# Kernel optimization log

Hardware: AMD Instinct MI355X
Metric: run time of the kernel (lower is better)

The kernel has to match this reference:

```python
import jax, jax.numpy as jnp
import numpy as np

DIM = 256
L = 16            # block_size (query rows per leaf block)
H = 8             # num_heads
D = DIM // H      # head_dim = 32
KC = L + 1        # key count: L leaf nodes + 1 block (mean) node, layout '16x17'
B = 2
N = 32768         # multiple of L -> no padding path
NB = N // L       # 2048 blocks
SCALE = D ** -0.5


def setup_inputs() -> dict:
    key = jax.random.key(0)
    ks = jax.random.split(key, 8)
    x = jax.random.normal(ks[0], (B, N, DIM), jnp.float32)
    attn_mask = jax.random.randint(ks[1], (NB, L, KC), 0, 2, dtype=jnp.int32)
    ar = jnp.arange(L)
    attn_mask = attn_mask.at[:, ar, ar].set(1)  # self always visible -> no all-masked rows
    edge_feats = jax.random.normal(ks[2], (NB, L, KC, 4), jnp.float32)
    s = DIM ** -0.5
    Wqkv = jax.random.normal(ks[3], (3 * DIM, DIM), jnp.float32) * s
    bqkv = jnp.zeros((3 * DIM,), jnp.float32)
    Wproj = jax.random.normal(ks[4], (DIM, DIM), jnp.float32) * s
    bproj = jnp.zeros((DIM,), jnp.float32)
    Wgate = jax.random.normal(ks[5], (H, 4), jnp.float32) * 0.01  # nn.init.normal_(std=0.01)
    bgate = jnp.zeros((H,), jnp.float32)
    return {"x": x, "attn_mask": attn_mask, "edge_feats": edge_feats,
            "Wqkv": Wqkv, "bqkv": bqkv, "Wproj": Wproj, "bproj": bproj,
            "Wgate": Wgate, "bgate": bgate}


def reference(x, attn_mask, edge_feats, Wqkv, bqkv, Wproj, bproj, Wgate, bgate):
    # x: [B, N, C] -> blocks [B, NB, L, C]
    x_blk = x.reshape(B, NB, L, DIM)
    block_node = x_blk.mean(axis=2, keepdims=True)           # virtual block node
    kv = jnp.concatenate([x_blk, block_node], axis=2)         # [B, NB, KC, C]

    # qkv projections (slice of the fused Linear; rows are independent so math is identical)
    q = x_blk @ Wqkv[:DIM].T + bqkv[:DIM]
    k = kv @ Wqkv[DIM:2 * DIM].T + bqkv[DIM:2 * DIM]
    v = kv @ Wqkv[2 * DIM:].T + bqkv[2 * DIM:]
    q = q.reshape(B, NB, L, H, D)
    k = k.reshape(B, NB, KC, H, D)
    v = v.reshape(B, NB, KC, H, D)

    scores = jnp.einsum('bnqhd,bnkhd->bnqkh', q, k) * SCALE   # [B, NB, L, KC, H]

    # physics bias: zero out + set channel 3 = 1 for block node column and self (diagonal)
    ar = jnp.arange(L)
    unit = jnp.array([0.0, 0.0, 0.0, 1.0], edge_feats.dtype)
    bias = edge_feats.at[:, :, L, :].set(unit)                # block-node column
    bias = bias.at[:, ar, ar, :].set(unit)                    # self bias on diagonal
    bias = jnp.broadcast_to(bias[None], (B, NB, L, KC, 4))    # expand over batch

    scores = scores + bias[..., 3:4]

    mask0 = (attn_mask[None] == 0)[..., None]                 # [1, NB, L, KC, 1]
    scores = jnp.where(mask0, -jnp.inf, scores)
    attn = jax.nn.softmax(scores, axis=3)

    gate = jnp.einsum('bnqkf,hf->bnqkh', bias, Wgate) + bgate  # edge-conditioned gate
    gate = jnp.where(mask0, 0.0, gate)

    combined = attn + gate
    out = jnp.einsum('bnqkh,bnkhd->bnqhd', combined, v).reshape(B, N, DIM)
    return out @ Wproj.T + bproj
```

## Files before the change

### kernel.cpp

```cpp
#include <hip/hip_runtime.h>
#include <cstdint>
#include <cstddef>

#define B_SZ 2
#define N_SEQ 32768
#define NB 2048
#define HD 32
#define LQ 16
#define KCNT 17
#define M_ROWS 65536
#define SCALE_F 0.17677669529663687f

typedef __attribute__((ext_vector_type(8))) short sv8;
typedef __attribute__((ext_vector_type(4))) short sv4;
typedef __attribute__((ext_vector_type(4))) float f4;

__device__ __forceinline__ short f2bf(float f) {
  unsigned u = __builtin_bit_cast(unsigned, f);
  u = (u + 0x7FFFu + ((u >> 16) & 1u)) >> 16;
  return (short)u;
}
__device__ __forceinline__ float bf2f(short s) {
  unsigned u = ((unsigned)(unsigned short)s) << 16;
  return __builtin_bit_cast(float, u);
}
__device__ __forceinline__ void gload16(const void* g, void* l) {
  __builtin_amdgcn_global_load_lds(
      (const __attribute__((address_space(1))) unsigned int*)g,
      (__attribute__((address_space(3))) unsigned int*)l, 16, 0, 0);
}
__device__ __forceinline__ f4 mfma16(sv8 a, sv8 b, f4 c) {
  return __builtin_amdgcn_mfma_f32_16x16x32_bf16(a, b, c, 0, 0, 0);
}

__global__ __launch_bounds__(256) void cast_w(
    const float* __restrict__ wq, const float* __restrict__ wp,
    short* __restrict__ W1, short* __restrict__ WP1) {
  const int i = blockIdx.x * 256 + threadIdx.x;
  const float* src;
  short* dst;
  int off;
  if (i < 49152) { src = wq; dst = W1; off = i; }
  else if (i < 49152 + 16384) { src = wp; dst = WP1; off = i - 49152; }
  else return;
  float4 v = ((const float4*)src)[off];
  sv4 h = {f2bf(v.x), f2bf(v.y), f2bf(v.z), f2bf(v.w)};
  *(sv4*)&dst[(size_t)off * 4] = h;
}

__global__ __launch_bounds__(256) void gemm_fused_qkv(
    const float* __restrict__ Xf, const short* __restrict__ B1,
    const float* __restrict__ bias, short* __restrict__ Qbf,
    short* __restrict__ Kbf, short* __restrict__ Vbf) {
  __shared__ __align__(16) short Ahs[2][128][32];
  __shared__ __align__(16) short Bhs[2][128][32];
  const int tid = threadIdx.x;
  const int w = tid >> 6, l = tid & 63;
  const int wm = w >> 1, wn = w & 1;
  const int bid = blockIdx.x;
  const int chunkc = (6 * 512) >> 3;
  const int lbid = (bid & 7) * chunkc + (bid >> 3);
  const int nti = lbid % 6, mti = lbid / 6;
  const int m0 = mti * 128, n0 = nti * 128;
  const int lr = l >> 2, lc = (l & 3) * 8;
  const int fr = l & 15, kg = (l >> 4) * 8;
  const int ar = w * 32 + lr, ac = lc;
  f4 acc[4][4] = {};

#pragma unroll
  for (int i = 0; i < 2; ++i)
    gload16(B1 + (size_t)(n0 + w * 32 + i * 16 + lr) * 256 + lc,
            (void*)&Bhs[0][w * 32 + i * 16][0]);
#pragma unroll
  for (int i = 0; i < 2; ++i) {
    const float* ap = Xf + (size_t)(m0 + ar + i * 16) * 256 + ac;
    float4 x0 = *(const float4*)ap;
    float4 x1 = *(const float4*)(ap + 4);
    sv8 o;
    o[0] = f2bf(x0.x); o[1] = f2bf(x0.y); o[2] = f2bf(x0.z); o[3] = f2bf(x0.w);
    o[4] = f2bf(x1.x); o[5] = f2bf(x1.y); o[6] = f2bf(x1.z); o[7] = f2bf(x1.w);
    *(sv8*)&Ahs[0][ar + i * 16][ac] = o;
  }
  asm volatile("s_waitcnt vmcnt(0) lgkmcnt(0)" ::: "memory");
  __builtin_amdgcn_s_barrier();

  for (int s = 0; s < 8; ++s) {
    const int cb = s & 1, nbuf = cb ^ 1;
    float4 pa0[2], pa1[2];
    if (s < 7) {
      const int sk = (s + 1) * 32;
#pragma unroll
      for (int i = 0; i < 2; ++i)
        gload16(B1 + (size_t)(n0 + w * 32 + i * 16 + lr) * 256 + sk + lc,
                (void*)&Bhs[nbuf][w * 32 + i * 16][0]);
#pragma unroll
      for (int i = 0; i < 2; ++i) {
        const float* ap = Xf + (size_t)(m0 + ar + i * 16) * 256 + sk + ac;
        pa0[i] = *(const float4*)ap;
        pa1[i] = *(const float4*)(ap + 4);
      }
    }
    sv8 fa[4], fb[4];
#pragma unroll
    for (int t = 0; t < 4; ++t) {
      fa[t] = *(const sv8*)&Ahs[cb][wm * 64 + t * 16 + fr][kg];
      fb[t] = *(const sv8*)&Bhs[cb][wn * 64 + t * 16 + fr][kg];
    }
#pragma unroll
    for (int mt = 0; mt < 4; ++mt)
#pragma unroll
      for (int nt2 = 0; nt2 < 4; ++nt2)
        acc[mt][nt2] = mfma16(fa[mt], fb[nt2], acc[mt][nt2]);
    if (s < 7) {
#pragma unroll
      for (int i = 0; i < 2; ++i) {
        sv8 o;
        o[0] = f2bf(pa0[i].x); o[1] = f2bf(pa0[i].y);
        o[2] = f2bf(pa0[i].z); o[3] = f2bf(pa0[i].w);
        o[4] = f2bf(pa1[i].x); o[5] = f2bf(pa1[i].y);
        o[6] = f2bf(pa1[i].z); o[7] = f2bf(pa1[i].w);
        *(sv8*)&Ahs[nbuf][ar + i * 16][ac] = o;
      }
    }
    asm volatile("s_waitcnt vmcnt(0) lgkmcnt(0)" ::: "memory");
    __builtin_amdgcn_s_barrier();
  }

  short* dst = (nti < 2) ? Qbf : ((nti < 4) ? Kbf : Vbf);
  const int r0 = (l >> 4) * 4;
#pragma unroll
  for (int mt = 0; mt < 4; ++mt)
#pragma unroll
    for (int nt2 = 0; nt2 < 4; ++nt2) {
      const int n = n0 + wn * 64 + nt2 * 16 + fr;
      const float bv = bias[n];
      const int nn = n & 255;
      const size_t mb = (size_t)(m0 + wm * 64 + mt * 16 + r0);
#pragma unroll
      for (int j = 0; j < 4; ++j)
        dst[(mb + j) * 256 + nn] = f2bf(acc[mt][nt2][j] + bv);
    }
}

__global__ __launch_bounds__(256) void gemm_proj1(
    const short* __restrict__ A1, const short* __restrict__ B1,
    const float* __restrict__ bias, float* __restrict__ C) {
  __shared__ __align__(16) short Ahs[2][128][32];
  __shared__ __align__(16) short Bhs[2][128][32];
  const int tid = threadIdx.x;
  const int w = tid >> 6, l = tid & 63;
  const int wm = w >> 1, wn = w & 1;
  const int bid = blockIdx.x;
  const int chunkc = (2 * 512) >> 3;
  const int lbid = (bid & 7) * chunkc + (bid >> 3);
  const int nti = lbid % 2, mti = lbid / 2;
  const int m0 = mti * 128, n0 = nti * 128;
  const int lr = l >> 2, lc = (l & 3) * 8;
  const int fr = l & 15, kg = (l >> 4) * 8;
  f4 acc[4][4] = {};
#pragma unroll
  for (int i = 0; i < 2; ++i) {
    const int row = w * 32 + i * 16;
    gload16(A1 + (size_t)(m0 + row + lr) * 256 + lc, (void*)&Ahs[0][row][0]);
    gload16(B1 + (size_t)(n0 + row + lr) * 256 + lc, (void*)&Bhs[0][row][0]);
  }
  asm volatile("s_waitcnt vmcnt(0)" ::: "memory");
  __builtin_amdgcn_s_barrier();
  int cur = 0;
  for (int s = 0; s < 8; ++s) {
    if (s < 7) {
      const int sk = (s + 1) * 32;
#pragma unroll
      for (int i = 0; i < 2; ++i) {
        const int row = w * 32 + i * 16;
        gload16(A1 + (size_t)(m0 + row + lr) * 256 + sk + lc,
                (void*)&Ahs[cur ^ 1][row][0]);
        gload16(B1 + (size_t)(n0 + row + lr) * 256 + sk + lc,
                (void*)&Bhs[cur ^ 1][row][0]);
      }
    }
    if (s > 0) {
      if (s < 7) asm volatile("s_waitcnt vmcnt(4)" ::: "memory");
      else asm volatile("s_waitcnt vmcnt(0)" ::: "memory");
      __builtin_amdgcn_s_barrier();
    }
    sv8 fa[4], fb[4];
#pragma unroll
    for (int t = 0; t < 4; ++t) {
      fa[t] = *(const sv8*)&Ahs[cur][wm * 64 + t * 16 + fr][kg];
      fb[t] = *(const sv8*)&Bhs[cur][wn * 64 + t * 16 + fr][kg];
    }
#pragma unroll
    for (int mt = 0; mt < 4; ++mt)
#pragma unroll
      for (int nt2 = 0; nt2 < 4; ++nt2)
        acc[mt][nt2] = mfma16(fa[mt], fb[nt2], acc[mt][nt2]);
    asm volatile("s_waitcnt lgkmcnt(0)" ::: "memory");
    __builtin_amdgcn_s_barrier();
    cur ^= 1;
  }
  const int r0 = (l >> 4) * 4;
#pragma unroll
  for (int mt = 0; mt < 4; ++mt)
#pragma unroll
    for (int nt2 = 0; nt2 < 4; ++nt2) {
      const int n = n0 + wn * 64 + nt2 * 16 + fr;
      const float bv = bias[n];
      const size_t mb = (size_t)(m0 + wm * 64 + mt * 16 + r0);
#pragma unroll
      for (int j = 0; j < 4; ++j) C[(mb + j) * 256 + n] = acc[mt][nt2][j] + bv;
    }
}

__global__ __launch_bounds__(256, 5) void attn_v7(
    const short* __restrict__ Qb, const short* __restrict__ Kb,
    const short* __restrict__ Vb, const int* __restrict__ amask,
    const float* __restrict__ efeat, const float* __restrict__ Wgate,
    const float* __restrict__ bgate, short* __restrict__ AO) {
  __shared__ __align__(16) short Kl[16 * 264];
  __shared__ __align__(16) short Vl[16 * 264];
  __shared__ __align__(16) short Ol[16 * 264];
  __shared__ float4 Es[LQ * KCNT];
  __shared__ int Ms[LQ * KCNT];

  const int tid = threadIdx.x, g = blockIdx.x;
  const int b = g >> 11, nb = g & (NB - 1);
  const size_t tok0 = (size_t)(b * N_SEQ + nb * LQ);
  const int w = tid >> 6, l = tid & 63;
  const int ln = l & 15, lg = l >> 4;
  const f4 fzero = {0.f, 0.f, 0.f, 0.f};

  sv8 qf[2];
#pragma unroll
  for (int hh = 0; hh < 2; ++hh) {
    const int h = w * 2 + hh;
    qf[hh] = *(const sv8*)(Qb + (tok0 + ln) * 256 + h * 32 + lg * 8);
  }

#pragma unroll
  for (int i = 0; i < 2; ++i) {
    const int f = tid + i * 256;
    const int t = f >> 5, c8 = (f & 31) * 8;
    *(sv8*)&Kl[t * 264 + c8] = *(const sv8*)(Kb + (tok0 + t) * 256 + c8);
    *(sv8*)&Vl[t * 264 + c8] = *(const sv8*)(Vb + (tok0 + t) * 256 + c8);
  }
  {
    const float4* esrc = (const float4*)(efeat + (size_t)nb * LQ * KCNT * 4);
    const int* msrc = amask + (size_t)nb * LQ * KCNT;
    Es[tid] = esrc[tid];
    Ms[tid] = msrc[tid];
    if (tid < LQ * KCNT - 256) {
      Es[256 + tid] = esrc[256 + tid];
      Ms[256 + tid] = msrc[256 + tid];
    }
  }
  __syncthreads();

  const int q = ln;
#pragma unroll
  for (int hh = 0; hh < 2; ++hh) {
    const int h = w * 2 + hh;
    sv8 ka = *(const sv8*)&Kl[ln * 264 + h * 32 + lg * 8];
    f4 sr = mfma16(ka, qf[hh], fzero);

    const float wg0 = Wgate[h * 4], wg1 = Wgate[h * 4 + 1];
    const float wg2 = Wgate[h * 4 + 2], wg3 = Wgate[h * 4 + 3];
    const float bg = bgate[h];

    float rs = sr[0] + sr[1] + sr[2] + sr[3];
    rs += __shfl_xor(rs, 16);
    rs += __shfl_xor(rs, 32);

    float s_[4], gt_[4];
    int vis_[4];
#pragma unroll
    for (int j = 0; j < 4; ++j) {
      const int kc = lg * 4 + j;
      float e0, e1, e2, e3;
      if (kc == q) { e0 = e1 = e2 = 0.f; e3 = 1.f; }
      else { float4 e = Es[q * KCNT + kc]; e0 = e.x; e1 = e.y; e2 = e.z; e3 = e.w; }
      const int m = Ms[q * KCNT + kc];
      vis_[j] = m;
      s_[j] = sr[j] * SCALE_F + e3;
      gt_[j] = m ? (e0 * wg0 + e1 * wg1 + e2 * wg2 + e3 * wg3 + bg) : 0.f;
    }
    const int m16 = Ms[q * KCNT + 16];
    const float s16 = rs * 0.0625f * SCALE_F + 1.0f;

    float mx = -1e30f;
#pragma unroll
    for (int j = 0; j < 4; ++j)
      if (vis_[j]) mx = fmaxf(mx, s_[j]);
    mx = fmaxf(mx, __shfl_xor(mx, 16));
    mx = fmaxf(mx, __shfl_xor(mx, 32));
    if (m16) mx = fmaxf(mx, s16);

    float p_[4], den = 0.f;
#pragma unroll
    for (int j = 0; j < 4; ++j) {
      p_[j] = vis_[j] ? __expf(s_[j] - mx) : 0.f;
      den += p_[j];
    }
    den += __shfl_xor(den, 16);
    den += __shfl_xor(den, 32);
    const float p16 = m16 ? __expf(s16 - mx) : 0.f;
    den += p16;
    const float inv = 1.f / den;
    const float gt16 = m16 ? (wg3 + bg) : 0.f;
    const float cb16 = (p16 * inv + gt16) * 0.0625f;
    float pc[4];
#pragma unroll
    for (int j = 0; j < 4; ++j) pc[j] = p_[j] * inv + gt_[j] + cb16;

    sv8 pa;
#pragma unroll
    for (int e = 0; e < 8; ++e) {
      const int kc = lg * 8 + e;
      const int src = ((kc >> 2) << 4) | q;
      const float v0 = __shfl(pc[e & 3], src);
      pa[e] = (kc < 16) ? f2bf(v0) : (short)0;
    }

#pragma unroll
    for (int t = 0; t < 2; ++t) {
      sv8 vb;
#pragma unroll
      for (int e = 0; e < 8; ++e) {
        const int vr = (lg * 8 + e) & 15;
        vb[e] = Vl[vr * 264 + h * 32 + t * 16 + ln];
      }
      f4 oacc = mfma16(pa, vb, fzero);
#pragma unroll
      for (int j = 0; j < 4; ++j)
        Ol[(lg * 4 + j) * 264 + h * 32 + t * 16 + ln] = f2bf(oacc[j]);
    }
  }
  __syncthreads();

#pragma unroll
  for (int i = 0; i < 2; ++i) {
    const int f = tid + i * 256;
    const int t = f >> 5, c8 = (f & 31) * 8;
    *(sv8*)(AO + (tok0 + t) * 256 + c8) = *(const sv8*)&Ol[t * 264 + c8];
  }
}

extern "C" void kernel_launch(void* const* d_in, const int* in_sizes, int n_in,
                              void* d_out, int out_size, void* d_ws, size_t ws_size,
                              hipStream_t stream) {
  const float* x = (const float*)d_in[0];
  const int* amask = (const int*)d_in[1];
  const float* efeat = (const float*)d_in[2];
  const float* Wqkv = (const float*)d_in[3];
  const float* bqkv = (const float*)d_in[4];
  const float* Wproj = (const float*)d_in[5];
  const float* bproj = (const float*)d_in[6];
  const float* Wgate = (const float*)d_in[7];
  const float* bgate = (const float*)d_in[8];
  float* out = (float*)d_out;

  char* ws = (char*)d_ws;
  const size_t QB_SZ = (size_t)M_ROWS * 256 * 2;
  const size_t W1_SZ = (size_t)768 * 256 * 2;
  const size_t WP1_SZ = (size_t)256 * 256 * 2;
  if (ws_size < 4 * QB_SZ + W1_SZ + WP1_SZ) return;

  short* Qbf = (short*)ws;
  short* Kbf = (short*)(ws + QB_SZ);
  short* Vbf = (short*)(ws + 2 * QB_SZ);
  short* AOh = (short*)(ws + 3 * QB_SZ);
  short* W1 = (short*)(ws + 4 * QB_SZ);
  short* WP1 = (short*)(ws + 4 * QB_SZ + W1_SZ);

  cast_w<<<dim3((49152 + 16384 + 255) / 256), 256, 0, stream>>>(Wqkv, Wproj,
                                                                W1, WP1);
  gemm_fused_qkv<<<dim3(6 * 512), 256, 0, stream>>>(x, W1, bqkv, Qbf, Kbf, Vbf);
  attn_v7<<<dim3(B_SZ * NB), 256, 0, stream>>>(Qbf, Kbf, Vbf, amask, efeat,
                                               Wgate, bgate, AOh);
  gemm_proj1<<<dim3(2 * 512), 256, 0, stream>>>(AOh, WP1, bproj, out);
}
```

Before: 138.5 us.

## Pre-cast x to bf16 and stage QKV GEMM epilogue through swizzled LDS

Converts x to bf16 in a separate cast pass so the QKV GEMM can load both operands with direct global-to-LDS loads. It also adds a finer-grained wait on outstanding loads, and writes outputs through an XOR-swizzled LDS tile so the global stores are coalesced 16-byte rows. The aim is to remove the per-stage float-to-bf16 conversion and register staging from the GEMM main loop and to avoid scattered 2-byte stores. The cost is an extra full pass that reads x in fp32 and writes a bf16 copy, plus more workspace. Since x is re-read six times by the GEMM, the extra pass may be partly offset by halved reads.

```diff
diff --git a/kernel.cpp b/kernel.cpp
--- a/kernel.cpp
+++ b/kernel.cpp
@@ -33,27 +33,28 @@
   return __builtin_amdgcn_mfma_f32_16x16x32_bf16(a, b, c, 0, 0, 0);
 }
 
-__global__ __launch_bounds__(256) void cast_w(
-    const float* __restrict__ wq, const float* __restrict__ wp,
+__global__ __launch_bounds__(256) void cast_all(
+    const float* __restrict__ x, const float* __restrict__ wq,
+    const float* __restrict__ wp, short* __restrict__ X1,
     short* __restrict__ W1, short* __restrict__ WP1) {
   const int i = blockIdx.x * 256 + threadIdx.x;
   const float* src;
   short* dst;
   int off;
-  if (i < 49152) { src = wq; dst = W1; off = i; }
-  else if (i < 49152 + 16384) { src = wp; dst = WP1; off = i - 49152; }
+  if (i < 4194304) { src = x; dst = X1; off = i; }
+  else if (i < 4194304 + 49152) { src = wq; dst = W1; off = i - 4194304; }
+  else if (i < 4194304 + 49152 + 16384) { src = wp; dst = WP1; off = i - 4194304 - 49152; }
   else return;
   float4 v = ((const float4*)src)[off];
   sv4 h = {f2bf(v.x), f2bf(v.y), f2bf(v.z), f2bf(v.w)};
   *(sv4*)&dst[(size_t)off * 4] = h;
 }
 
-__global__ __launch_bounds__(256) void gemm_fused_qkv(
-    const float* __restrict__ Xf, const short* __restrict__ B1,
+__global__ __launch_bounds__(256) void gemm_bf_qkv(
+    const short* __restrict__ A1, const short* __restrict__ B1,
     const float* __restrict__ bias, short* __restrict__ Qbf,
     short* __restrict__ Kbf, short* __restrict__ Vbf) {
-  __shared__ __align__(16) short Ahs[2][128][32];
-  __shared__ __align__(16) short Bhs[2][128][32];
+  __shared__ __align__(16) short LB[2][2][128][32];
   const int tid = threadIdx.x;
   const int w = tid >> 6, l = tid & 63;
   const int wm = w >> 1, wn = w & 1;
@@ -64,82 +65,72 @@
   const int m0 = mti * 128, n0 = nti * 128;
   const int lr = l >> 2, lc = (l & 3) * 8;
   const int fr = l & 15, kg = (l >> 4) * 8;
-  const int ar = w * 32 + lr, ac = lc;
   f4 acc[4][4] = {};
-
-#pragma unroll
-  for (int i = 0; i < 2; ++i)
-    gload16(B1 + (size_t)(n0 + w * 32 + i * 16 + lr) * 256 + lc,
-            (void*)&Bhs[0][w * 32 + i * 16][0]);
 #pragma unroll
   for (int i = 0; i < 2; ++i) {
-    const float* ap = Xf + (size_t)(m0 + ar + i * 16) * 256 + ac;
-    float4 x0 = *(const float4*)ap;
-    float4 x1 = *(const float4*)(ap + 4);
-    sv8 o;
-    o[0] = f2bf(x0.x); o[1] = f2bf(x0.y); o[2] = f2bf(x0.z); o[3] = f2bf(x0.w);
-    o[4] = f2bf(x1.x); o[5] = f2bf(x1.y); o[6] = f2bf(x1.z); o[7] = f2bf(x1.w);
-    *(sv8*)&Ahs[0][ar + i * 16][ac] = o;
-  }
-  asm volatile("s_waitcnt vmcnt(0) lgkmcnt(0)" ::: "memory");
+    const int row = w * 32 + i * 16;
+    gload16(A1 + (size_t)(m0 + row + lr) * 256 + lc, (void*)&LB[0][0][row][0]);
+    gload16(B1 + (size_t)(n0 + row + lr) * 256 + lc, (void*)&LB[0][1][row][0]);
+  }
+  asm volatile("s_waitcnt vmcnt(0)" ::: "memory");
   __builtin_amdgcn_s_barrier();
-
+  int cur = 0;
   for (int s = 0; s < 8; ++s) {
-    const int cb = s & 1, nbuf = cb ^ 1;
-    float4 pa0[2], pa1[2];
     if (s < 7) {
       const int sk = (s + 1) * 32;
 #pragma unroll
-      for (int i = 0; i < 2; ++i)
-        gload16(B1 + (size_t)(n0 + w * 32 + i * 16 + lr) * 256 + sk + lc,
-                (void*)&Bhs[nbuf][w * 32 + i * 16][0]);
-#pragma unroll
       for (int i = 0; i < 2; ++i) {
-        const float* ap = Xf + (size_t)(m0 + ar + i * 16) * 256 + sk + ac;
-        pa0[i] = *(const float4*)ap;
-        pa1[i] = *(const float4*)(ap + 4);
+        const int row = w * 32 + i * 16;
+        gload16(A1 + (size_t)(m0 + row + lr) * 256 + sk + lc,
+                (void*)&LB[cur ^ 1][0][row][0]);
+        gload16(B1 + (size_t)(n0 + row + lr) * 256 + sk + lc,
+                (void*)&LB[cur ^ 1][1][row][0]);
       }
     }
+    if (s > 0) {
+      if (s < 7) asm volatile("s_waitcnt vmcnt(4)" ::: "memory");
+      else asm volatile("s_waitcnt vmcnt(0)" ::: "memory");
+      __builtin_amdgcn_s_barrier();
+    }
     sv8 fa[4], fb[4];
 #pragma unroll
     for (int t = 0; t < 4; ++t) {
-      fa[t] = *(const sv8*)&Ahs[cb][wm * 64 + t * 16 + fr][kg];
-      fb[t] = *(const sv8*)&Bhs[cb][wn * 64 + t * 16 + fr][kg];
+      fa[t] = *(const sv8*)&LB[cur][0][wm * 64 + t * 16 + fr][kg];
+      fb[t] = *(const sv8*)&LB[cur][1][wn * 64 + t * 16 + fr][kg];
     }
 #pragma unroll
     for (int mt = 0; mt < 4; ++mt)
 #pragma unroll
       for (int nt2 = 0; nt2 < 4; ++nt2)
         acc[mt][nt2] = mfma16(fa[mt], fb[nt2], acc[mt][nt2]);
-    if (s < 7) {
-#pragma unroll
-      for (int i = 0; i < 2; ++i) {
-        sv8 o;
-        o[0] = f2bf(pa0[i].x); o[1] = f2bf(pa0[i].y);
-        o[2] = f2bf(pa0[i].z); o[3] = f2bf(pa0[i].w);
-        o[4] = f2bf(pa1[i].x); o[5] = f2bf(pa1[i].y);
-        o[6] = f2bf(pa1[i].z); o[7] = f2bf(pa1[i].w);
-        *(sv8*)&Ahs[nbuf][ar + i * 16][ac] = o;
+    asm volatile("s_waitcnt lgkmcnt(0)" ::: "memory");
+    __builtin_amdgcn_s_barrier();
+    cur ^= 1;
+  }
+  short* Lout = &LB[0][0][0][0];
+  const int r0 = (l >> 4) * 4;
+#pragma unroll
+  for (int mt = 0; mt < 4; ++mt)
+#pragma unroll
+    for (int nt2 = 0; nt2 < 4; ++nt2) {
+      const int n = wn * 64 + nt2 * 16 + fr;
+      const float bv = bias[n0 + n];
+#pragma unroll
+      for (int j = 0; j < 4; ++j) {
+        const int m = wm * 64 + mt * 16 + r0 + j;
+        Lout[m * 128 + (n ^ ((m & 7) << 3))] = f2bf(acc[mt][nt2][j] + bv);
       }
     }
-    asm volatile("s_waitcnt vmcnt(0) lgkmcnt(0)" ::: "memory");
-    __builtin_amdgcn_s_barrier();
-  }
-
+  __builtin_amdgcn_s_barrier();
   short* dst = (nti < 2) ? Qbf : ((nti < 4) ? Kbf : Vbf);
-  const int r0 = (l >> 4) * 4;
-#pragma unroll
-  for (int mt = 0; mt < 4; ++mt)
-#pragma unroll
-    for (int nt2 = 0; nt2 < 4; ++nt2) {
-      const int n = n0 + wn * 64 + nt2 * 16 + fr;
-      const float bv = bias[n];
-      const int nn = n & 255;
-      const size_t mb = (size_t)(m0 + wm * 64 + mt * 16 + r0);
-#pragma unroll
-      for (int j = 0; j < 4; ++j)
-        dst[(mb + j) * 256 + nn] = f2bf(acc[mt][nt2][j] + bv);
-    }
+  const int nnb = (nti & 1) * 128;
+  const int rrow = tid >> 4, seg = (tid & 15) * 8;
+#pragma unroll
+  for (int p = 0; p < 8; ++p) {
+    const int row = p * 16 + rrow;
+    sv8 v = *(const sv8*)&Lout[row * 128 + (seg ^ ((row & 7) << 3))];
+    *(sv8*)&dst[(size_t)(m0 + row) * 256 + nnb + seg] = v;
+  }
 }
 
 __global__ __launch_bounds__(256) void gemm_proj1(
@@ -363,18 +354,20 @@
   const size_t QB_SZ = (size_t)M_ROWS * 256 * 2;
   const size_t W1_SZ = (size_t)768 * 256 * 2;
   const size_t WP1_SZ = (size_t)256 * 256 * 2;
-  if (ws_size < 4 * QB_SZ + W1_SZ + WP1_SZ) return;
-
-  short* Qbf = (short*)ws;
-  short* Kbf = (short*)(ws + QB_SZ);
-  short* Vbf = (short*)(ws + 2 * QB_SZ);
-  short* AOh = (short*)(ws + 3 * QB_SZ);
-  short* W1 = (short*)(ws + 4 * QB_SZ);
-  short* WP1 = (short*)(ws + 4 * QB_SZ + W1_SZ);
-
-  cast_w<<<dim3((49152 + 16384 + 255) / 256), 256, 0, stream>>>(Wqkv, Wproj,
-                                                                W1, WP1);
-  gemm_fused_qkv<<<dim3(6 * 512), 256, 0, stream>>>(x, W1, bqkv, Qbf, Kbf, Vbf);
+  if (ws_size < 5 * QB_SZ + W1_SZ + WP1_SZ) return;
+
+  short* X1 = (short*)ws;
+  short* Qbf = (short*)(ws + QB_SZ);
+  short* Kbf = (short*)(ws + 2 * QB_SZ);
+  short* Vbf = (short*)(ws + 3 * QB_SZ);
+  short* AOh = (short*)(ws + 4 * QB_SZ);
+  short* W1 = (short*)(ws + 5 * QB_SZ);
+  short* WP1 = (short*)(ws + 5 * QB_SZ + W1_SZ);
+
+  const int total_f4 = 4194304 + 49152 + 16384;
+  cast_all<<<dim3((total_f4 + 255) / 256), 256, 0, stream>>>(x, Wqkv, Wproj,
+                                                             X1, W1, WP1);
+  gemm_bf_qkv<<<dim3(6 * 512), 256, 0, stream>>>(X1, W1, bqkv, Qbf, Kbf, Vbf);
   attn_v7<<<dim3(B_SZ * NB), 256, 0, stream>>>(Qbf, Kbf, Vbf, amask, efeat,
                                                Wgate, bgate, AOh);
   gemm_proj1<<<dim3(2 * 512), 256, 0, stream>>>(AOh, WP1, bproj, out);
```

Result: faster. 122.8 us (-11.3%).

## Stage QKV GEMM epilogue through swizzled LDS and shrink attention LDS footprint

Applied to the files above, without the earlier changes.

The fused QKV GEMM now writes its bf16 outputs through an XOR-swizzled LDS tile and stores 16-byte row segments to global memory, replacing scattered 2-byte stores. Its prologue and main loop issue the X loads before the B loads, and scheduling barriers pin the order of global loads, MFMAs and conversions. The attention kernel reuses the K buffer for its output tile after computing all scores up front, which drops one LDS array so the launch bound can rise to 7 blocks per CU. It also remaps block IDs for locality. The risks are an extra barrier and LDS round trip in the GEMM epilogue, and extra register pressure in attention from holding both score tiles live.

```diff
diff --git a/kernel.cpp b/kernel.cpp
--- a/kernel.cpp
+++ b/kernel.cpp
@@ -52,8 +52,7 @@
     const float* __restrict__ Xf, const short* __restrict__ B1,
     const float* __restrict__ bias, short* __restrict__ Qbf,
     short* __restrict__ Kbf, short* __restrict__ Vbf) {
-  __shared__ __align__(16) short Ahs[2][128][32];
-  __shared__ __align__(16) short Bhs[2][128][32];
+  __shared__ __align__(16) short LB[2][2][128][32];
   const int tid = threadIdx.x;
   const int w = tid >> 6, l = tid & 63;
   const int wm = w >> 1, wn = w & 1;
@@ -67,79 +66,99 @@
   const int ar = w * 32 + lr, ac = lc;
   f4 acc[4][4] = {};
 
-#pragma unroll
-  for (int i = 0; i < 2; ++i)
-    gload16(B1 + (size_t)(n0 + w * 32 + i * 16 + lr) * 256 + lc,
-            (void*)&Bhs[0][w * 32 + i * 16][0]);
-#pragma unroll
-  for (int i = 0; i < 2; ++i) {
-    const float* ap = Xf + (size_t)(m0 + ar + i * 16) * 256 + ac;
-    float4 x0 = *(const float4*)ap;
-    float4 x1 = *(const float4*)(ap + 4);
-    sv8 o;
-    o[0] = f2bf(x0.x); o[1] = f2bf(x0.y); o[2] = f2bf(x0.z); o[3] = f2bf(x0.w);
-    o[4] = f2bf(x1.x); o[5] = f2bf(x1.y); o[6] = f2bf(x1.z); o[7] = f2bf(x1.w);
-    *(sv8*)&Ahs[0][ar + i * 16][ac] = o;
+  {
+    float4 xa[2][2];
+#pragma unroll
+    for (int i = 0; i < 2; ++i) {
+      const float* ap = Xf + (size_t)(m0 + ar + i * 16) * 256 + ac;
+      xa[i][0] = *(const float4*)ap;
+      xa[i][1] = *(const float4*)(ap + 4);
+    }
+#pragma unroll
+    for (int i = 0; i < 2; ++i)
+      gload16(B1 + (size_t)(n0 + w * 32 + i * 16 + lr) * 256 + lc,
+              (void*)&LB[0][1][w * 32 + i * 16][0]);
+#pragma unroll
+    for (int i = 0; i < 2; ++i) {
+      sv8 o;
+      o[0] = f2bf(xa[i][0].x); o[1] = f2bf(xa[i][0].y);
+      o[2] = f2bf(xa[i][0].z); o[3] = f2bf(xa[i][0].w);
+      o[4] = f2bf(xa[i][1].x); o[5] = f2bf(xa[i][1].y);
+      o[6] = f2bf(xa[i][1].z); o[7] = f2bf(xa[i][1].w);
+      *(sv8*)&LB[0][0][ar + i * 16][ac] = o;
+    }
   }
   asm volatile("s_waitcnt vmcnt(0) lgkmcnt(0)" ::: "memory");
   __builtin_amdgcn_s_barrier();
 
   for (int s = 0; s < 8; ++s) {
     const int cb = s & 1, nbuf = cb ^ 1;
-    float4 pa0[2], pa1[2];
+    float4 xa[2][2];
     if (s < 7) {
       const int sk = (s + 1) * 32;
 #pragma unroll
+      for (int i = 0; i < 2; ++i) {
+        const float* ap = Xf + (size_t)(m0 + ar + i * 16) * 256 + sk + ac;
+        xa[i][0] = *(const float4*)ap;
+        xa[i][1] = *(const float4*)(ap + 4);
+      }
+#pragma unroll
       for (int i = 0; i < 2; ++i)
         gload16(B1 + (size_t)(n0 + w * 32 + i * 16 + lr) * 256 + sk + lc,
-                (void*)&Bhs[nbuf][w * 32 + i * 16][0]);
-#pragma unroll
-      for (int i = 0; i < 2; ++i) {
-        const float* ap = Xf + (size_t)(m0 + ar + i * 16) * 256 + sk + ac;
-        pa0[i] = *(const float4*)ap;
-        pa1[i] = *(const float4*)(ap + 4);
-      }
-    }
+                (void*)&LB[nbuf][1][w * 32 + i * 16][0]);
+    }
+    __builtin_amdgcn_sched_barrier(0);
     sv8 fa[4], fb[4];
 #pragma unroll
     for (int t = 0; t < 4; ++t) {
-      fa[t] = *(const sv8*)&Ahs[cb][wm * 64 + t * 16 + fr][kg];
-      fb[t] = *(const sv8*)&Bhs[cb][wn * 64 + t * 16 + fr][kg];
+      fa[t] = *(const sv8*)&LB[cb][0][wm * 64 + t * 16 + fr][kg];
+      fb[t] = *(const sv8*)&LB[cb][1][wn * 64 + t * 16 + fr][kg];
     }
 #pragma unroll
     for (int mt = 0; mt < 4; ++mt)
 #pragma unroll
       for (int nt2 = 0; nt2 < 4; ++nt2)
         acc[mt][nt2] = mfma16(fa[mt], fb[nt2], acc[mt][nt2]);
+    __builtin_amdgcn_sched_barrier(0);
     if (s < 7) {
 #pragma unroll
       for (int i = 0; i < 2; ++i) {
         sv8 o;
-        o[0] = f2bf(pa0[i].x); o[1] = f2bf(pa0[i].y);
-        o[2] = f2bf(pa0[i].z); o[3] = f2bf(pa0[i].w);
-        o[4] = f2bf(pa1[i].x); o[5] = f2bf(pa1[i].y);
-        o[6] = f2bf(pa1[i].z); o[7] = f2bf(pa1[i].w);
-        *(sv8*)&Ahs[nbuf][ar + i * 16][ac] = o;
+        o[0] = f2bf(xa[i][0].x); o[1] = f2bf(xa[i][0].y);
+        o[2] = f2bf(xa[i][0].z); o[3] = f2bf(xa[i][0].w);
+        o[4] = f2bf(xa[i][1].x); o[5] = f2bf(xa[i][1].y);
+        o[6] = f2bf(xa[i][1].z); o[7] = f2bf(xa[i][1].w);
+        *(sv8*)&LB[nbuf][0][ar + i * 16][ac] = o;
       }
     }
     asm volatile("s_waitcnt vmcnt(0) lgkmcnt(0)" ::: "memory");
     __builtin_amdgcn_s_barrier();
   }
 
+  short* Lout = &LB[0][0][0][0];
+  const int r0 = (l >> 4) * 4;
+#pragma unroll
+  for (int mt = 0; mt < 4; ++mt)
+#pragma unroll
+    for (int nt2 = 0; nt2 < 4; ++nt2) {
+      const int n = wn * 64 + nt2 * 16 + fr;
+      const float bv = bias[n0 + n];
+#pragma unroll
+      for (int j = 0; j < 4; ++j) {
+        const int m = wm * 64 + mt * 16 + r0 + j;
+        Lout[m * 128 + (n ^ ((m & 7) << 3))] = f2bf(acc[mt][nt2][j] + bv);
+      }
+    }
+  __builtin_amdgcn_s_barrier();
   short* dst = (nti < 2) ? Qbf : ((nti < 4) ? Kbf : Vbf);
-  const int r0 = (l >> 4) * 4;
-#pragma unroll
-  for (int mt = 0; mt < 4; ++mt)
-#pragma unroll
-    for (int nt2 = 0; nt2 < 4; ++nt2) {
-      const int n = n0 + wn * 64 + nt2 * 16 + fr;
-      const float bv = bias[n];
-      const int nn = n & 255;
-      const size_t mb = (size_t)(m0 + wm * 64 + mt * 16 + r0);
-#pragma unroll
-      for (int j = 0; j < 4; ++j)
-        dst[(mb + j) * 256 + nn] = f2bf(acc[mt][nt2][j] + bv);
-    }
+  const int nnb = (nti & 1) * 128;
+  const int rrow = tid >> 4, seg = (tid & 15) * 8;
+#pragma unroll
+  for (int p = 0; p < 8; ++p) {
+    const int row = p * 16 + rrow;
+    sv8 v = *(const sv8*)&Lout[row * 128 + (seg ^ ((row & 7) << 3))];
+    *(sv8*)&dst[(size_t)(m0 + row) * 256 + nnb + seg] = v;
+  }
 }
 
 __global__ __launch_bounds__(256) void gemm_proj1(
@@ -212,18 +231,20 @@
     }
 }
 
-__global__ __launch_bounds__(256, 5) void attn_v7(
+__global__ __launch_bounds__(256, 7) void attn_v8(
     const short* __restrict__ Qb, const short* __restrict__ Kb,
     const short* __restrict__ Vb, const int* __restrict__ amask,
     const float* __restrict__ efeat, const float* __restrict__ Wgate,
     const float* __restrict__ bgate, short* __restrict__ AO) {
   __shared__ __align__(16) short Kl[16 * 264];
   __shared__ __align__(16) short Vl[16 * 264];
-  __shared__ __align__(16) short Ol[16 * 264];
   __shared__ float4 Es[LQ * KCNT];
   __shared__ int Ms[LQ * KCNT];
-
-  const int tid = threadIdx.x, g = blockIdx.x;
+  short* Ol = Kl;
+
+  const int tid = threadIdx.x;
+  const int bid = blockIdx.x;
+  const int g = (bid & 7) * 512 + (bid >> 3);
   const int b = g >> 11, nb = g & (NB - 1);
   const size_t tok0 = (size_t)(b * N_SEQ + nb * LQ);
   const int w = tid >> 6, l = tid & 63;
@@ -257,11 +278,16 @@
   __syncthreads();
 
   const int q = ln;
+  sv8 ka0 = *(const sv8*)&Kl[ln * 264 + (w * 2 + 0) * 32 + lg * 8];
+  sv8 ka1 = *(const sv8*)&Kl[ln * 264 + (w * 2 + 1) * 32 + lg * 8];
+  const f4 sr0 = mfma16(ka0, qf[0], fzero);
+  const f4 sr1 = mfma16(ka1, qf[1], fzero);
+  __syncthreads();
+
 #pragma unroll
   for (int hh = 0; hh < 2; ++hh) {
     const int h = w * 2 + hh;
-    sv8 ka = *(const sv8*)&Kl[ln * 264 + h * 32 + lg * 8];
-    f4 sr = mfma16(ka, qf[hh], fzero);
+    const f4 sr = (hh == 0) ? sr0 : sr1;
 
     const float wg0 = Wgate[h * 4], wg1 = Wgate[h * 4 + 1];
     const float wg2 = Wgate[h * 4 + 2], wg3 = Wgate[h * 4 + 3];
@@ -375,7 +401,7 @@
   cast_w<<<dim3((49152 + 16384 + 255) / 256), 256, 0, stream>>>(Wqkv, Wproj,
                                                                 W1, WP1);
   gemm_fused_qkv<<<dim3(6 * 512), 256, 0, stream>>>(x, W1, bqkv, Qbf, Kbf, Vbf);
-  attn_v7<<<dim3(B_SZ * NB), 256, 0, stream>>>(Qbf, Kbf, Vbf, amask, efeat,
+  attn_v8<<<dim3(B_SZ * NB), 256, 0, stream>>>(Qbf, Kbf, Vbf, amask, efeat,
                                                Wgate, bgate, AOh);
   gemm_proj1<<<dim3(2 * 512), 256, 0, stream>>>(AOh, WP1, bproj, out);
 }
```

Result: no change. 136.3 us (-1.6%).
